# Optimization experiments

Hardware: AMD Instinct MI355X
Metric: run time of the kernel (lower is better)

The kernel has to match this reference:

```python
import jax, jax.numpy as jnp
import numpy as np

B, T, D, H, OUT = 1024, 2048, 5, 64, 128


def _lstm_layer(x, Wih, Whh, bih, bhh):
    """PyTorch-convention LSTM layer. x: [B,T,Din]; gate order i,f,g,o."""
    b, t = x.shape[0], x.shape[1]
    h = Whh.shape[1]
    # Precompute input projections for all timesteps (the only big GEMM).
    xp = jnp.einsum('btd,gd->btg', x, Wih) + bih + bhh        # [B,T,4H]
    xp = jnp.swapaxes(xp, 0, 1)                               # [T,B,4H]

    def step(carry, xt):
        hprev, cprev = carry
        gates = xt + hprev @ Whh.T                            # [B,4H]
        i, f, g, o = jnp.split(gates, 4, axis=-1)
        i = jax.nn.sigmoid(i)
        f = jax.nn.sigmoid(f)
        g = jnp.tanh(g)
        o = jax.nn.sigmoid(o)
        c = f * cprev + i * g
        hnew = o * jnp.tanh(c)
        return (hnew, c), hnew

    h0 = jnp.zeros((b, h), x.dtype)
    (hT, cT), hs = jax.lax.scan(step, (h0, h0), xp)
    return jnp.swapaxes(hs, 0, 1), hT                         # [B,T,H], [B,H]


def setup_inputs() -> dict:
    key = jax.random.key(0)
    ks = jax.random.split(key, 11)
    s = 1.0 / np.sqrt(H)  # PyTorch LSTM init range

    def u(k, shape):
        return jax.random.uniform(k, shape, jnp.float32, -s, s)

    return {
        'x': jax.random.normal(ks[0], (B, T, D), jnp.float32),
        'W_ih0': u(ks[1], (4 * H, D)),
        'W_hh0': u(ks[2], (4 * H, H)),
        'b_ih0': u(ks[3], (4 * H,)),
        'b_hh0': u(ks[4], (4 * H,)),
        'W_ih1': u(ks[5], (4 * H, H)),
        'W_hh1': u(ks[6], (4 * H, H)),
        'b_ih1': u(ks[7], (4 * H,)),
        'b_hh1': u(ks[8], (4 * H,)),
        'W_fc': u(ks[9], (OUT, H)),
        'b_fc': u(ks[10], (OUT,)),
    }


def reference(x, W_ih0, W_hh0, b_ih0, b_hh0, W_ih1, W_hh1, b_ih1, b_hh1, W_fc, b_fc):
    # Layer 1 over raw 5-dim signal; inter-layer dropout is inactive at inference.
    y1, _ = _lstm_layer(x, W_ih0, W_hh0, b_ih0, b_hh0)
    # Layer 2; only its final hidden state hn[-1] is used downstream.
    _, h2 = _lstm_layer(y1, W_ih1, W_hh1, b_ih1, b_hh1)
    return jax.nn.relu(h2 @ W_fc.T + b_fc)                    # [B,128]
```

## Files before the change

kernel.cpp:

```cpp
#include <hip/hip_runtime.h>
#include <math.h>

#define BATCH 1024
#define TSEQ  2048
#define DIN   5
#define H     64
#define BT    4
#define SSTR  144
#define NOUT  128

typedef _Float16 f16x8 __attribute__((ext_vector_type(8)));
typedef float    f32x4 __attribute__((ext_vector_type(4)));

#if __has_builtin(__builtin_amdgcn_rcpf)
__device__ __forceinline__ float rcp_fast(float x) { return __builtin_amdgcn_rcpf(x); }
#else
__device__ __forceinline__ float rcp_fast(float x) { return 1.0f / x; }
#endif

#define LOG2E 1.44269504088896f
#define MFMA16(A, B, C) __builtin_amdgcn_mfma_f32_16x16x32_f16((A), (B), (C), 0, 0, 0)

__device__ __forceinline__ float sigm2(float s) {
    return rcp_fast(1.0f + __builtin_amdgcn_exp2f(-s));
}
__device__ __forceinline__ float tanh2(float s) {
    return fmaf(-2.0f, rcp_fast(__builtin_amdgcn_exp2f(s) + 1.0f), 1.0f);
}

__device__ __forceinline__ void sync_lgkm() {
    asm volatile("s_waitcnt lgkmcnt(0)" ::: "memory");
    __builtin_amdgcn_s_barrier();
    asm volatile("" ::: "memory");
}

__global__ __launch_bounds__(512)
void lstm_mfma(const float* __restrict__ x,
               const float* __restrict__ Wih0, const float* __restrict__ Whh0,
               const float* __restrict__ bih0, const float* __restrict__ bhh0,
               const float* __restrict__ Wih1, const float* __restrict__ Whh1,
               const float* __restrict__ bih1, const float* __restrict__ bhh1,
               const float* __restrict__ Wfc,  const float* __restrict__ bfc,
               float* __restrict__ out)
{
    __shared__ alignas(16) _Float16 S[2][BT * SSTR];
    __shared__ alignas(16) float    h2f[BT][H];

    const int tid  = threadIdx.x;
    const int w    = tid >> 6;
    const int lane = tid & 63;
    const int col  = lane & 15;
    const int q    = lane >> 4;
    const int ww   = w & 3;
    const int lay  = w >> 2;
    const int hu   = 16 * ww + col;
    const int b0   = blockIdx.x * BT;

    for (int j = tid; j < 2 * BT * SSTR; j += 512)
        ((_Float16*)S)[j] = (_Float16)0.0f;

    const float sgl[4] = {LOG2E, LOG2E, 2.0f * LOG2E, LOG2E};

    f16x8 Bf[4][4];
    f32x4 bC[4];
    float wx[4][DIN];
    float b1s[4];
    #pragma unroll
    for (int g = 0; g < 4; ++g) {
        const int   row = g * 64 + hu;
        const float sg  = sgl[g];
        if (lay) {
            const float* wa = Wih1 + row * H;
            const float* wb = Whh1 + row * H;
            #pragma unroll
            for (int j = 0; j < 8; ++j) {
                const int k = q * 8 + j;
                Bf[g][0][j] = (_Float16)(wa[k]      * sg);
                Bf[g][1][j] = (_Float16)(wa[32 + k] * sg);
                Bf[g][2][j] = (_Float16)(wb[k]      * sg);
                Bf[g][3][j] = (_Float16)(wb[32 + k] * sg);
            }
            const float bb = (bih1[row] + bhh1[row]) * sg;
            bC[g] = f32x4{bb, bb, bb, bb};
        } else {
            const float* wh = Whh0 + row * H;
            #pragma unroll
            for (int j = 0; j < 8; ++j) {
                const int k = q * 8 + j;
                Bf[g][0][j] = (_Float16)(wh[k]      * sg);
                Bf[g][1][j] = (_Float16)(wh[32 + k] * sg);
            }
            #pragma unroll
            for (int j = 0; j < DIN; ++j)
                wx[g][j] = Wih0[row * DIN + j] * sg;
            b1s[g] = (bih0[row] + bhh0[row]) * sg;
        }
    }

    const float* xq = x + (size_t)(b0 + q) * TSEQ * DIN;
    float x0 = 0.f, x1 = 0.f, x2 = 0.f, x3 = 0.f, x4 = 0.f;
    float dxs[4] = {0.f, 0.f, 0.f, 0.f};
    if (lay == 0) {
        float a0 = xq[0], a1 = xq[1], a2 = xq[2], a3 = xq[3], a4 = xq[4];
        #pragma unroll
        for (int g = 0; g < 4; ++g) {
            float s = fmaf(a0, wx[g][0], b1s[g]);
            s = fmaf(a1, wx[g][1], s);
            s = fmaf(a2, wx[g][2], s);
            s = fmaf(a3, wx[g][3], s);
            dxs[g] = fmaf(a4, wx[g][4], s);
        }
        x0 = xq[DIN + 0]; x1 = xq[DIN + 1]; x2 = xq[DIN + 2];
        x3 = xq[DIN + 3]; x4 = xq[DIN + 4];
        xq += 2 * DIN;
    }

    const int ab  = (col >> 2) * SSTR + q * 8;
    const int wb1 = q * SSTR + hu;
    const int wb2 = q * SSTR + 64 + hu;
    float cst = 0.0f, h2fin = 0.0f;

    __syncthreads();

    #pragma unroll 1
    for (int i = 0; i <= TSEQ; ++i) {
        const _Float16* rb   = S[(i + 1) & 1];
        _Float16*       wbuf = S[i & 1];

        if (lay == 0) {
            const bool ld2 = (i + 2 < TSEQ);
            float n0, n1, n2, n3, n4;
            if (ld2) { n0 = xq[0]; n1 = xq[1]; n2 = xq[2]; n3 = xq[3]; n4 = xq[4]; xq += DIN; }

            f16x8 a0 = *(const f16x8*)&rb[ab];
            f16x8 a1 = *(const f16x8*)&rb[ab + 32];

            f32x4 d[4];
            __builtin_amdgcn_s_setprio(1);
            #pragma unroll
            for (int g = 0; g < 4; ++g) {
                f32x4 c0 = {dxs[g], 0.f, 0.f, 0.f};
                d[g] = MFMA16(a0, Bf[g][0], c0);
                d[g] = MFMA16(a1, Bf[g][1], d[g]);
            }
            __builtin_amdgcn_s_setprio(0);

            if (i < TSEQ) {
                float iv = sigm2(d[0][0]);
                float fv = sigm2(d[1][0]);
                float gv = tanh2(d[2][0]);
                float ov = sigm2(d[3][0]);
                cst = fmaf(fv, cst, iv * gv);
                wbuf[wb1] = (_Float16)(ov * tanh2(2.0f * LOG2E * cst));
            }
            if (i + 1 < TSEQ) {
                #pragma unroll
                for (int g = 0; g < 4; ++g) {
                    float s = fmaf(x0, wx[g][0], b1s[g]);
                    s = fmaf(x1, wx[g][1], s);
                    s = fmaf(x2, wx[g][2], s);
                    s = fmaf(x3, wx[g][3], s);
                    dxs[g] = fmaf(x4, wx[g][4], s);
                }
            }
            if (ld2) { x0 = n0; x1 = n1; x2 = n2; x3 = n3; x4 = n4; }
        } else {
            f16x8 ay0 = *(const f16x8*)&rb[ab];
            f16x8 ay1 = *(const f16x8*)&rb[ab + 32];
            f16x8 ah0 = *(const f16x8*)&rb[ab + 64];
            f16x8 ah1 = *(const f16x8*)&rb[ab + 96];
            f32x4 e[4], f[4];
            const f32x4 z4 = {0.f, 0.f, 0.f, 0.f};
            __builtin_amdgcn_s_setprio(1);
            #pragma unroll
            for (int g = 0; g < 4; ++g) {
                e[g] = MFMA16(ay0, Bf[g][0], bC[g]);
                e[g] = MFMA16(ay1, Bf[g][1], e[g]);
                f[g] = MFMA16(ah0, Bf[g][2], z4);
                f[g] = MFMA16(ah1, Bf[g][3], f[g]);
            }
            __builtin_amdgcn_s_setprio(0);
            if (i > 0) {
                float p0 = e[0][0] + f[0][0];
                float p1 = e[1][0] + f[1][0];
                float p2 = e[2][0] + f[2][0];
                float p3 = e[3][0] + f[3][0];
                float iv = sigm2(p0);
                float fv = sigm2(p1);
                float gv = tanh2(p2);
                float ov = sigm2(p3);
                cst = fmaf(fv, cst, iv * gv);
                h2fin = ov * tanh2(2.0f * LOG2E * cst);
                wbuf[wb2] = (_Float16)h2fin;
            }
        }
        sync_lgkm();
    }

    if (lay) h2f[q][hu] = h2fin;
    __syncthreads();
    {
        const int e = tid >> 7;
        const int o = tid & (NOUT - 1);
        const float4* wr = (const float4*)(Wfc + o * H);
        const float*  hv = h2f[e];
        float s0 = 0.f, s1 = 0.f, s2 = 0.f, s3 = 0.f;
        #pragma unroll
        for (int k = 0; k < H / 4; ++k) {
            float4 wv = wr[k];
            s0 = fmaf(wv.x, hv[4 * k + 0], s0);
            s1 = fmaf(wv.y, hv[4 * k + 1], s1);
            s2 = fmaf(wv.z, hv[4 * k + 2], s2);
            s3 = fmaf(wv.w, hv[4 * k + 3], s3);
        }
        float acc = bfc[o] + (s0 + s1) + (s2 + s3);
        out[(size_t)(b0 + e) * NOUT + o] = fmaxf(acc, 0.0f);
    }
}

extern "C" void kernel_launch(void* const* d_in, const int* in_sizes, int n_in,
                              void* d_out, int out_size, void* d_ws, size_t ws_size,
                              hipStream_t stream) {
    const float* x    = (const float*)d_in[0];
    const float* Wih0 = (const float*)d_in[1];
    const float* Whh0 = (const float*)d_in[2];
    const float* bih0 = (const float*)d_in[3];
    const float* bhh0 = (const float*)d_in[4];
    const float* Wih1 = (const float*)d_in[5];
    const float* Whh1 = (const float*)d_in[6];
    const float* bih1 = (const float*)d_in[7];
    const float* bhh1 = (const float*)d_in[8];
    const float* Wfc  = (const float*)d_in[9];
    const float* bfc  = (const float*)d_in[10];
    float* out = (float*)d_out;

    lstm_mfma<<<dim3(BATCH / BT), dim3(512), 0, stream>>>(
        x, Wih0, Whh0, bih0, bhh0, Wih1, Whh1, bih1, bhh1, Wfc, bfc, out);
}
```

Measured before the change: 1.029 ms.

## Replace per-step block barrier with LDS flag handshakes and 4-deep buffers

Drops the block-wide barrier at every timestep. Layer-0 and layer-1 wavefronts now coordinate through per-wave progress counters in shared memory, spin-waiting with s_sleep, and the hidden-state buffer ring grows from 2 to 4 slots so layer 0 can run up to a few steps ahead of layer 1. This aims to decouple the two layers and remove barrier stalls from the serial recurrence. The cost is polling overhead, memory-ordering risk in the flag protocol (no explicit fence beyond the lgkmcnt wait), and possible slowdown if the spin loops add latency.

```diff
diff --git a/kernel.cpp b/kernel.cpp
--- a/kernel.cpp
+++ b/kernel.cpp
@@ -8,6 +8,7 @@
 #define BT    4
 #define SSTR  144
 #define NOUT  128
+#define NBUF  4
 
 typedef _Float16 f16x8 __attribute__((ext_vector_type(8)));
 typedef float    f32x4 __attribute__((ext_vector_type(4)));
@@ -28,9 +29,23 @@
     return fmaf(-2.0f, rcp_fast(__builtin_amdgcn_exp2f(s) + 1.0f), 1.0f);
 }
 
-__device__ __forceinline__ void sync_lgkm() {
+__device__ __forceinline__ int min4v(volatile const int* fl) {
+    int a = fl[0]; int b = fl[1]; int c = fl[2]; int d = fl[3];
+    return min(min(a, b), min(c, d));
+}
+__device__ __forceinline__ void wait_ge(volatile const int* fl, int tgt) {
+    while (min4v(fl) < tgt) __builtin_amdgcn_s_sleep(1);
+    asm volatile("" ::: "memory");
+}
+__device__ __forceinline__ void wait2_ge(volatile const int* f1, int t1,
+                                         volatile const int* f2, int t2) {
+    while (min4v(f1) < t1 || min4v(f2) < t2) __builtin_amdgcn_s_sleep(1);
+    asm volatile("" ::: "memory");
+}
+__device__ __forceinline__ void publish(volatile int* slot, int v, bool lead) {
     asm volatile("s_waitcnt lgkmcnt(0)" ::: "memory");
-    __builtin_amdgcn_s_barrier();
+    __builtin_amdgcn_sched_barrier(0);
+    if (lead) *slot = v;
     asm volatile("" ::: "memory");
 }
 
@@ -43,8 +58,9 @@
                const float* __restrict__ Wfc,  const float* __restrict__ bfc,
                float* __restrict__ out)
 {
-    __shared__ alignas(16) _Float16 S[2][BT * SSTR];
+    __shared__ alignas(16) _Float16 S[NBUF][BT * SSTR];
     __shared__ alignas(16) float    h2f[BT][H];
+    __shared__ alignas(16) int      flg[8];
 
     const int tid  = threadIdx.x;
     const int w    = tid >> 6;
@@ -56,8 +72,10 @@
     const int hu   = 16 * ww + col;
     const int b0   = blockIdx.x * BT;
 
-    for (int j = tid; j < 2 * BT * SSTR; j += 512)
+    for (int j = tid; j < NBUF * BT * SSTR; j += 512)
         ((_Float16*)S)[j] = (_Float16)0.0f;
+    if (tid < 4)      flg[tid] = -1;
+    else if (tid < 8) flg[tid] = 0;
 
     const float sgl[4] = {LOG2E, LOG2E, 2.0f * LOG2E, LOG2E};
 
@@ -120,17 +138,22 @@
     const int wb2 = q * SSTR + 64 + hu;
     float cst = 0.0f, h2fin = 0.0f;
 
+    volatile int* w1fl = flg;
+    volatile int* w2fl = flg + 4;
+
     __syncthreads();
 
-    #pragma unroll 1
-    for (int i = 0; i <= TSEQ; ++i) {
-        const _Float16* rb   = S[(i + 1) & 1];
-        _Float16*       wbuf = S[i & 1];
-
-        if (lay == 0) {
+    if (lay == 0) {
+        #pragma unroll 1
+        for (int i = 0; i < TSEQ; ++i) {
+            const _Float16* rb   = S[(i + 3) & 3];
+            _Float16*       wbuf = S[i & 3];
+
             const bool ld2 = (i + 2 < TSEQ);
             float n0, n1, n2, n3, n4;
             if (ld2) { n0 = xq[0]; n1 = xq[1]; n2 = xq[2]; n3 = xq[3]; n4 = xq[4]; xq += DIN; }
+
+            wait_ge(w1fl, i - 1);
 
             f16x8 a0 = *(const f16x8*)&rb[ab];
             f16x8 a1 = *(const f16x8*)&rb[ab + 32];
@@ -145,14 +168,13 @@
             }
             __builtin_amdgcn_s_setprio(0);
 
-            if (i < TSEQ) {
-                float iv = sigm2(d[0][0]);
-                float fv = sigm2(d[1][0]);
-                float gv = tanh2(d[2][0]);
-                float ov = sigm2(d[3][0]);
-                cst = fmaf(fv, cst, iv * gv);
-                wbuf[wb1] = (_Float16)(ov * tanh2(2.0f * LOG2E * cst));
-            }
+            float iv = sigm2(d[0][0]);
+            float fv = sigm2(d[1][0]);
+            float gv = tanh2(d[2][0]);
+            float ov = sigm2(d[3][0]);
+            cst = fmaf(fv, cst, iv * gv);
+            const float hval = ov * tanh2(2.0f * LOG2E * cst);
+
             if (i + 1 < TSEQ) {
                 #pragma unroll
                 for (int g = 0; g < 4; ++g) {
@@ -164,11 +186,24 @@
                 }
             }
             if (ld2) { x0 = n0; x1 = n1; x2 = n2; x3 = n3; x4 = n4; }
-        } else {
+
+            wait_ge(w2fl, i - 3);
+            wbuf[wb1] = (_Float16)hval;
+            publish(&w1fl[ww], i, lane == 0);
+        }
+    } else {
+        #pragma unroll 1
+        for (int i = 1; i <= TSEQ; ++i) {
+            const _Float16* rb   = S[(i + 3) & 3];
+            _Float16*       wbuf = S[i & 3];
+
+            wait2_ge(w1fl, i - 1, w2fl, i - 1);
+
             f16x8 ay0 = *(const f16x8*)&rb[ab];
             f16x8 ay1 = *(const f16x8*)&rb[ab + 32];
             f16x8 ah0 = *(const f16x8*)&rb[ab + 64];
             f16x8 ah1 = *(const f16x8*)&rb[ab + 96];
+
             f32x4 e[4], f[4];
             const f32x4 z4 = {0.f, 0.f, 0.f, 0.f};
             __builtin_amdgcn_s_setprio(1);
@@ -180,21 +215,21 @@
                 f[g] = MFMA16(ah1, Bf[g][3], f[g]);
             }
             __builtin_amdgcn_s_setprio(0);
-            if (i > 0) {
-                float p0 = e[0][0] + f[0][0];
-                float p1 = e[1][0] + f[1][0];
-                float p2 = e[2][0] + f[2][0];
-                float p3 = e[3][0] + f[3][0];
-                float iv = sigm2(p0);
-                float fv = sigm2(p1);
-                float gv = tanh2(p2);
-                float ov = sigm2(p3);
-                cst = fmaf(fv, cst, iv * gv);
-                h2fin = ov * tanh2(2.0f * LOG2E * cst);
-                wbuf[wb2] = (_Float16)h2fin;
-            }
-        }
-        sync_lgkm();
+
+            float p0 = e[0][0] + f[0][0];
+            float p1 = e[1][0] + f[1][0];
+            float p2 = e[2][0] + f[2][0];
+            float p3 = e[3][0] + f[3][0];
+            float iv = sigm2(p0);
+            float fv = sigm2(p1);
+            float gv = tanh2(p2);
+            float ov = sigm2(p3);
+            cst = fmaf(fv, cst, iv * gv);
+            h2fin = ov * tanh2(2.0f * LOG2E * cst);
+
+            wbuf[wb2] = (_Float16)h2fin;
+            publish(&w2fl[ww], i, lane == 0);
+        }
     }
 
     if (lay) h2f[q][hu] = h2fin;
```

After: 1.491 ms. +44.9%, slower.

## Move layer-2 input projection to layer-1 waves, pass via LDS with extra pipeline stage

Applied to the files above, without the earlier changes.

The layer-2 input projection (Wih1·h1 plus bias) is now computed by the layer-1 waves from the h1 they just read, and handed to the layer-2 waves through a double-buffered LDS array. This shortens layer 2's critical path per step to only the recurrent Whh1 MFMAs plus activations, balancing MFMA work between the two wave groups. The loop gains one extra step of pipeline latency, and the layer-1 waves now carry more MFMAs and registers. Launch bounds also request two blocks per CU.

```diff
diff --git a/kernel.cpp b/kernel.cpp
--- a/kernel.cpp
+++ b/kernel.cpp
@@ -34,7 +34,7 @@
     asm volatile("" ::: "memory");
 }
 
-__global__ __launch_bounds__(512)
+__global__ __launch_bounds__(512, 2)
 void lstm_mfma(const float* __restrict__ x,
                const float* __restrict__ Wih0, const float* __restrict__ Whh0,
                const float* __restrict__ bih0, const float* __restrict__ bhh0,
@@ -45,6 +45,7 @@
 {
     __shared__ alignas(16) _Float16 S[2][BT * SSTR];
     __shared__ alignas(16) float    h2f[BT][H];
+    __shared__ alignas(16) float4   E[2][4][64];
 
     const int tid  = threadIdx.x;
     const int w    = tid >> 6;
@@ -61,8 +62,9 @@
 
     const float sgl[4] = {LOG2E, LOG2E, 2.0f * LOG2E, LOG2E};
 
-    f16x8 Bf[4][4];
-    f32x4 bC[4];
+    f16x8 Bf[4][2];
+    f16x8 Cf[4][2];
+    f32x4 bC2[4];
     float wx[4][DIN];
     float b1s[4];
     #pragma unroll
@@ -70,30 +72,30 @@
         const int   row = g * 64 + hu;
         const float sg  = sgl[g];
         if (lay) {
-            const float* wa = Wih1 + row * H;
             const float* wb = Whh1 + row * H;
             #pragma unroll
             for (int j = 0; j < 8; ++j) {
                 const int k = q * 8 + j;
-                Bf[g][0][j] = (_Float16)(wa[k]      * sg);
-                Bf[g][1][j] = (_Float16)(wa[32 + k] * sg);
-                Bf[g][2][j] = (_Float16)(wb[k]      * sg);
-                Bf[g][3][j] = (_Float16)(wb[32 + k] * sg);
-            }
-            const float bb = (bih1[row] + bhh1[row]) * sg;
-            bC[g] = f32x4{bb, bb, bb, bb};
+                Bf[g][0][j] = (_Float16)(wb[k]      * sg);
+                Bf[g][1][j] = (_Float16)(wb[32 + k] * sg);
+            }
         } else {
             const float* wh = Whh0 + row * H;
+            const float* wi = Wih1 + row * H;
             #pragma unroll
             for (int j = 0; j < 8; ++j) {
                 const int k = q * 8 + j;
                 Bf[g][0][j] = (_Float16)(wh[k]      * sg);
                 Bf[g][1][j] = (_Float16)(wh[32 + k] * sg);
+                Cf[g][0][j] = (_Float16)(wi[k]      * sg);
+                Cf[g][1][j] = (_Float16)(wi[32 + k] * sg);
             }
             #pragma unroll
             for (int j = 0; j < DIN; ++j)
                 wx[g][j] = Wih0[row * DIN + j] * sg;
             b1s[g] = (bih0[row] + bhh0[row]) * sg;
+            const float bb2 = (bih1[row] + bhh1[row]) * sg;
+            bC2[g] = f32x4{bb2, bb2, bb2, bb2};
         }
     }
 
@@ -123,29 +125,43 @@
     __syncthreads();
 
     #pragma unroll 1
-    for (int i = 0; i <= TSEQ; ++i) {
+    for (int i = 0; i <= TSEQ + 1; ++i) {
         const _Float16* rb   = S[(i + 1) & 1];
         _Float16*       wbuf = S[i & 1];
 
         if (lay == 0) {
-            const bool ld2 = (i + 2 < TSEQ);
+            const bool dact = (i < TSEQ);
+            const bool eact = (i >= 1) && (i <= TSEQ);
+            const bool ld2  = (i + 2 < TSEQ);
             float n0, n1, n2, n3, n4;
             if (ld2) { n0 = xq[0]; n1 = xq[1]; n2 = xq[2]; n3 = xq[3]; n4 = xq[4]; xq += DIN; }
 
-            f16x8 a0 = *(const f16x8*)&rb[ab];
-            f16x8 a1 = *(const f16x8*)&rb[ab + 32];
-
-            f32x4 d[4];
+            f16x8 a0, a1;
+            if (dact || eact) {
+                a0 = *(const f16x8*)&rb[ab];
+                a1 = *(const f16x8*)&rb[ab + 32];
+            }
+
+            f32x4 d[4], e[4];
             __builtin_amdgcn_s_setprio(1);
-            #pragma unroll
-            for (int g = 0; g < 4; ++g) {
-                f32x4 c0 = {dxs[g], 0.f, 0.f, 0.f};
-                d[g] = MFMA16(a0, Bf[g][0], c0);
-                d[g] = MFMA16(a1, Bf[g][1], d[g]);
+            if (dact) {
+                #pragma unroll
+                for (int g = 0; g < 4; ++g) {
+                    f32x4 c0 = {dxs[g], 0.f, 0.f, 0.f};
+                    d[g] = MFMA16(a0, Bf[g][0], c0);
+                    d[g] = MFMA16(a1, Bf[g][1], d[g]);
+                }
+            }
+            if (eact) {
+                #pragma unroll
+                for (int g = 0; g < 4; ++g) {
+                    e[g] = MFMA16(a0, Cf[g][0], bC2[g]);
+                    e[g] = MFMA16(a1, Cf[g][1], e[g]);
+                }
             }
             __builtin_amdgcn_s_setprio(0);
 
-            if (i < TSEQ) {
+            if (dact) {
                 float iv = sigm2(d[0][0]);
                 float fv = sigm2(d[1][0]);
                 float gv = tanh2(d[2][0]);
@@ -164,35 +180,34 @@
                 }
             }
             if (ld2) { x0 = n0; x1 = n1; x2 = n2; x3 = n3; x4 = n4; }
-        } else {
-            f16x8 ay0 = *(const f16x8*)&rb[ab];
-            f16x8 ay1 = *(const f16x8*)&rb[ab + 32];
+            if (eact)
+                E[i & 1][ww][lane] = float4{e[0][0], e[1][0], e[2][0], e[3][0]};
+        } else if (i >= 2) {
             f16x8 ah0 = *(const f16x8*)&rb[ab + 64];
             f16x8 ah1 = *(const f16x8*)&rb[ab + 96];
-            f32x4 e[4], f[4];
+            float4 er = E[(i + 1) & 1][ww][lane];
+
+            f32x4 f[4];
             const f32x4 z4 = {0.f, 0.f, 0.f, 0.f};
             __builtin_amdgcn_s_setprio(1);
             #pragma unroll
             for (int g = 0; g < 4; ++g) {
-                e[g] = MFMA16(ay0, Bf[g][0], bC[g]);
-                e[g] = MFMA16(ay1, Bf[g][1], e[g]);
-                f[g] = MFMA16(ah0, Bf[g][2], z4);
-                f[g] = MFMA16(ah1, Bf[g][3], f[g]);
+                f[g] = MFMA16(ah0, Bf[g][0], z4);
+                f[g] = MFMA16(ah1, Bf[g][1], f[g]);
             }
             __builtin_amdgcn_s_setprio(0);
-            if (i > 0) {
-                float p0 = e[0][0] + f[0][0];
-                float p1 = e[1][0] + f[1][0];
-                float p2 = e[2][0] + f[2][0];
-                float p3 = e[3][0] + f[3][0];
-                float iv = sigm2(p0);
-                float fv = sigm2(p1);
-                float gv = tanh2(p2);
-                float ov = sigm2(p3);
-                cst = fmaf(fv, cst, iv * gv);
-                h2fin = ov * tanh2(2.0f * LOG2E * cst);
-                wbuf[wb2] = (_Float16)h2fin;
-            }
+
+            float p0 = er.x + f[0][0];
+            float p1 = er.y + f[1][0];
+            float p2 = er.z + f[2][0];
+            float p3 = er.w + f[3][0];
+            float iv = sigm2(p0);
+            float fv = sigm2(p1);
+            float gv = tanh2(p2);
+            float ov = sigm2(p3);
+            cst = fmaf(fv, cst, iv * gv);
+            h2fin = ov * tanh2(2.0f * LOG2E * cst);
+            wbuf[wb2] = (_Float16)h2fin;
         }
         sync_lgkm();
     }
```

New measurement: 1.215 ms. 1.18x slower.

## Stagger LSTM layer phases so MFMA and activations of both layers alternate

Applied to the files above, without the earlier changes.

Each timestep is split into two barrier-separated phases. Layer‑0 warps issue their MFMAs while layer‑1 warps evaluate activations from the previous step, and then the roles swap. Layer‑1 now accumulates all four MFMAs into one chain, and the loop runs one extra iteration to drain the pipeline. The aim is to stop both layers contending for the matrix units at the same moment. The cost is a second workgroup barrier per timestep and a longer dependent MFMA chain for layer 1.

```diff
diff --git a/kernel.cpp b/kernel.cpp
--- a/kernel.cpp
+++ b/kernel.cpp
@@ -120,78 +120,84 @@
     const int wb2 = q * SSTR + 64 + hu;
     float cst = 0.0f, h2fin = 0.0f;
 
+    f32x4 d[4];
+    f32x4 d2[4];
+
     __syncthreads();
 
     #pragma unroll 1
-    for (int i = 0; i <= TSEQ; ++i) {
-        const _Float16* rb   = S[(i + 1) & 1];
-        _Float16*       wbuf = S[i & 1];
+    for (int i = 0; i <= TSEQ + 1; ++i) {
+        float n0, n1, n2, n3, n4;
+        bool ld2 = false;
 
         if (lay == 0) {
-            const bool ld2 = (i + 2 < TSEQ);
-            float n0, n1, n2, n3, n4;
-            if (ld2) { n0 = xq[0]; n1 = xq[1]; n2 = xq[2]; n3 = xq[3]; n4 = xq[4]; xq += DIN; }
-
-            f16x8 a0 = *(const f16x8*)&rb[ab];
-            f16x8 a1 = *(const f16x8*)&rb[ab + 32];
-
-            f32x4 d[4];
-            __builtin_amdgcn_s_setprio(1);
-            #pragma unroll
-            for (int g = 0; g < 4; ++g) {
-                f32x4 c0 = {dxs[g], 0.f, 0.f, 0.f};
-                d[g] = MFMA16(a0, Bf[g][0], c0);
-                d[g] = MFMA16(a1, Bf[g][1], d[g]);
-            }
-            __builtin_amdgcn_s_setprio(0);
-
+            if (i < TSEQ) {
+                ld2 = (i + 2 < TSEQ);
+                if (ld2) { n0 = xq[0]; n1 = xq[1]; n2 = xq[2]; n3 = xq[3]; n4 = xq[4]; xq += DIN; }
+
+                const _Float16* rb = S[(i + 1) & 1];
+                f16x8 a0 = *(const f16x8*)&rb[ab];
+                f16x8 a1 = *(const f16x8*)&rb[ab + 32];
+                __builtin_amdgcn_s_setprio(1);
+                #pragma unroll
+                for (int g = 0; g < 4; ++g) {
+                    f32x4 c0 = {dxs[g], 0.f, 0.f, 0.f};
+                    d[g] = MFMA16(a0, Bf[g][0], c0);
+                    d[g] = MFMA16(a1, Bf[g][1], d[g]);
+                }
+                __builtin_amdgcn_s_setprio(0);
+            }
+        } else {
+            if (i >= 2) {
+                float iv = sigm2(d2[0][0]);
+                float fv = sigm2(d2[1][0]);
+                float gv = tanh2(d2[2][0]);
+                float ov = sigm2(d2[3][0]);
+                cst = fmaf(fv, cst, iv * gv);
+                h2fin = ov * tanh2(2.0f * LOG2E * cst);
+                S[i & 1][wb2] = (_Float16)h2fin;
+            }
+        }
+        sync_lgkm();
+
+        if (lay == 0) {
             if (i < TSEQ) {
                 float iv = sigm2(d[0][0]);
                 float fv = sigm2(d[1][0]);
                 float gv = tanh2(d[2][0]);
                 float ov = sigm2(d[3][0]);
                 cst = fmaf(fv, cst, iv * gv);
-                wbuf[wb1] = (_Float16)(ov * tanh2(2.0f * LOG2E * cst));
-            }
-            if (i + 1 < TSEQ) {
+                S[i & 1][wb1] = (_Float16)(ov * tanh2(2.0f * LOG2E * cst));
+
+                if (i + 1 < TSEQ) {
+                    #pragma unroll
+                    for (int g = 0; g < 4; ++g) {
+                        float s = fmaf(x0, wx[g][0], b1s[g]);
+                        s = fmaf(x1, wx[g][1], s);
+                        s = fmaf(x2, wx[g][2], s);
+                        s = fmaf(x3, wx[g][3], s);
+                        dxs[g] = fmaf(x4, wx[g][4], s);
+                    }
+                }
+                if (ld2) { x0 = n0; x1 = n1; x2 = n2; x3 = n3; x4 = n4; }
+            }
+        } else {
+            if (i >= 1 && i <= TSEQ) {
+                const _Float16* rby = S[(i + 1) & 1];
+                const _Float16* rbh = S[i & 1];
+                f16x8 ay0 = *(const f16x8*)&rby[ab];
+                f16x8 ay1 = *(const f16x8*)&rby[ab + 32];
+                f16x8 ah0 = *(const f16x8*)&rbh[ab + 64];
+                f16x8 ah1 = *(const f16x8*)&rbh[ab + 96];
+                __builtin_amdgcn_s_setprio(1);
                 #pragma unroll
                 for (int g = 0; g < 4; ++g) {
-                    float s = fmaf(x0, wx[g][0], b1s[g]);
-                    s = fmaf(x1, wx[g][1], s);
-                    s = fmaf(x2, wx[g][2], s);
-                    s = fmaf(x3, wx[g][3], s);
-                    dxs[g] = fmaf(x4, wx[g][4], s);
+                    d2[g] = MFMA16(ay0, Bf[g][0], bC[g]);
+                    d2[g] = MFMA16(ay1, Bf[g][1], d2[g]);
+                    d2[g] = MFMA16(ah0, Bf[g][2], d2[g]);
+                    d2[g] = MFMA16(ah1, Bf[g][3], d2[g]);
                 }
-            }
-            if (ld2) { x0 = n0; x1 = n1; x2 = n2; x3 = n3; x4 = n4; }
-        } else {
-            f16x8 ay0 = *(const f16x8*)&rb[ab];
-            f16x8 ay1 = *(const f16x8*)&rb[ab + 32];
-            f16x8 ah0 = *(const f16x8*)&rb[ab + 64];
-            f16x8 ah1 = *(const f16x8*)&rb[ab + 96];
-            f32x4 e[4], f[4];
-            const f32x4 z4 = {0.f, 0.f, 0.f, 0.f};
-            __builtin_amdgcn_s_setprio(1);
-            #pragma unroll
-            for (int g = 0; g < 4; ++g) {
-                e[g] = MFMA16(ay0, Bf[g][0], bC[g]);
-                e[g] = MFMA16(ay1, Bf[g][1], e[g]);
-                f[g] = MFMA16(ah0, Bf[g][2], z4);
-                f[g] = MFMA16(ah1, Bf[g][3], f[g]);
-            }
-            __builtin_amdgcn_s_setprio(0);
-            if (i > 0) {
-                float p0 = e[0][0] + f[0][0];
-                float p1 = e[1][0] + f[1][0];
-                float p2 = e[2][0] + f[2][0];
-                float p3 = e[3][0] + f[3][0];
-                float iv = sigm2(p0);
-                float fv = sigm2(p1);
-                float gv = tanh2(p2);
-                float ov = sigm2(p3);
-                cst = fmaf(fv, cst, iv * gv);
-                h2fin = ov * tanh2(2.0f * LOG2E * cst);
-                wbuf[wb2] = (_Float16)h2fin;
+                __builtin_amdgcn_s_setprio(0);
             }
         }
         sync_lgkm();
```

Result: slower. 1.240 ms (+20.5%).
